# Optimization experiments

Hardware: AMD Instinct MI355X
Metric: run time of the kernel (lower is better)

The kernel has to match this reference:

```python
import jax, jax.numpy as jnp
import numpy as np

S, B, H = 2048, 16, 512      # seq_len, batch, hidden_size
L = 4096                     # total labels across batch
SMAX = 16                    # max span length
LAB = 256                    # label_size
V = 32000                    # len(voc)


def setup_inputs() -> dict:
    key = jax.random.key(0)
    ks = jax.random.split(key, 10)
    hidden = jax.random.normal(ks[0], (S, B, H), jnp.float32)
    begins = jax.random.randint(ks[1], (L,), 1, S - SMAX - 1)          # >=1 so begin-1 valid
    lens = jax.random.randint(ks[2], (L,), 1, SMAX + 1)                # span length in [1, SMAX]
    ends = begins + lens                                               # < S so hidden[end] valid
    bids = jax.random.randint(ks[3], (L,), 0, B)
    tags = jax.random.randint(ks[4], (L,), 0, V)
    sc = 0.02
    W1 = jax.random.normal(ks[5], (3 * H, LAB), jnp.float32) * sc
    b1 = jnp.zeros((LAB,), jnp.float32)
    W2 = jax.random.normal(ks[6], (LAB, LAB), jnp.float32) * sc
    b2 = jnp.zeros((LAB,), jnp.float32)
    Wo = jax.random.normal(ks[7], (LAB, V), jnp.float32) * sc
    bo = jnp.zeros((V,), jnp.float32)
    return dict(hidden=hidden, begins=begins, ends=ends, bids=bids, tags=tags,
                W1=W1, b1=b1, W2=W2, b2=b2, Wo=Wo, bo=bo)


def reference(hidden, begins, ends, bids, tags, W1, b1, W2, b2, Wo, bo):
    # --- batched span embed: gather + masked mean + boundary concat ---
    pos = begins[:, None] + jnp.arange(SMAX)            # [L, SMAX]
    valid = (pos < ends[:, None]).astype(hidden.dtype)  # [L, SMAX]
    posc = jnp.minimum(pos, S - 1)
    g = hidden[posc, bids[:, None]]                     # [L, SMAX, H] gather
    span_len = (ends - begins).astype(hidden.dtype)[:, None]
    mean = (g * valid[..., None]).sum(axis=1) / span_len           # [L, H]
    left = hidden[begins - 1, bids]                                 # [L, H]
    right = hidden[ends, bids]                                      # [L, H]
    span_emb = jnp.concatenate([left, mean, right], axis=-1)        # [L, 3H]
    # --- hidden2feature: Linear -> sigmoid -> Linear (dropout = eval identity) ---
    feat = jax.nn.sigmoid(span_emb @ W1 + b1) @ W2 + b2             # [L, LAB]
    # --- SoftmaxLoss: -log_softmax(h2o(feat)).gather(tags).mean() per label ---
    logp = jax.nn.log_softmax(feat @ Wo + bo, axis=-1)              # [L, V]
    per_label = -logp[jnp.arange(L), tags]                          # one tag per label
    return per_label.sum() / (L + 1e-5)
```

## Files before the change

kernel.cpp:

```cpp
#include <hip/hip_runtime.h>
#include <math.h>

#define S 2048
#define B 16
#define H 512
#define L 4096
#define SMAX 16
#define LAB 256
#define V 32000
#define NCH 250
#define LOG2E 1.44269504f

typedef __attribute__((ext_vector_type(8))) short short8;
typedef __attribute__((ext_vector_type(4))) float float4v;

__device__ inline ushort f2bf(float x) {
  union { float f; unsigned u; } c; c.f = x;
  unsigned r = c.u + 0x7fffu + ((c.u >> 16) & 1u);
  return (ushort)(r >> 16);
}
__device__ inline float bf2f(ushort h) {
  union { unsigned u; float f; } c; c.u = ((unsigned)h) << 16;
  return c.f;
}

__global__ __launch_bounds__(256) void spanb_kernel(
    const float* __restrict__ hidden, const int* __restrict__ begins,
    const int* __restrict__ ends, const int* __restrict__ bids,
    ushort* __restrict__ spanb) {
  int sub = threadIdx.x >> 7, t = threadIdx.x & 127;
  int l = blockIdx.x * 2 + sub;
  int b = bids[l], s0 = begins[l], s1 = ends[l];
  const float4* hidv = (const float4*)hidden;
  float4 lf = hidv[((size_t)(s0 - 1) * B + b) * 128 + t];
  float4 rf = hidv[((size_t)s1 * B + b) * 128 + t];
  float4 m = make_float4(0.f, 0.f, 0.f, 0.f);
  int len = s1 - s0;
  for (int j = 0; j < len; ++j) {
    float4 g = hidv[((size_t)(s0 + j) * B + b) * 128 + t];
    m.x += g.x; m.y += g.y; m.z += g.z; m.w += g.w;
  }
  float inv = 1.0f / (float)len;
  ushort* sp = spanb + (size_t)l * 1536;
  ushort4 u;
  u.x = f2bf(lf.x); u.y = f2bf(lf.y); u.z = f2bf(lf.z); u.w = f2bf(lf.w);
  *(ushort4*)&sp[t * 4] = u;
  u.x = f2bf(m.x * inv); u.y = f2bf(m.y * inv);
  u.z = f2bf(m.z * inv); u.w = f2bf(m.w * inv);
  *(ushort4*)&sp[512 + t * 4] = u;
  u.x = f2bf(rf.x); u.y = f2bf(rf.y); u.z = f2bf(rf.z); u.w = f2bf(rf.w);
  *(ushort4*)&sp[1024 + t * 4] = u;
}

__global__ __launch_bounds__(256) void tcast_kernel(
    const float* __restrict__ src, ushort* __restrict__ dst, int K, int N) {
  __shared__ ushort tile[64 * 72];
  int t = threadIdx.x;
  int n0 = blockIdx.x * 64;
  int k0 = blockIdx.y * 64;
  #pragma unroll
  for (int p = 0; p < 16; ++p) {
    int k = p * 4 + (t >> 6);
    int n = t & 63;
    tile[n * 72 + k] = f2bf(src[(size_t)(k0 + k) * N + n0 + n]);
  }
  __syncthreads();
  #pragma unroll
  for (int p = 0; p < 2; ++p) {
    int idx = p * 256 + t;
    int n = idx >> 3, c = idx & 7;
    *(uint4*)&dst[(size_t)(n0 + n) * K + k0 + c * 8] =
        *(const uint4*)&tile[n * 72 + c * 8];
  }
}

#define FST 72
__global__ __launch_bounds__(256, 2) void feat_mfma_kernel(
    const ushort* __restrict__ spanb, const ushort* __restrict__ W1b,
    const float* __restrict__ b1, const ushort* __restrict__ W2b,
    const float* __restrict__ b2, ushort* __restrict__ featb) {
  __shared__ ushort As[32 * FST];
  __shared__ ushort Bs[256 * FST];
  __shared__ ushort Hs[32 * 264];
  int tid = threadIdx.x;
  int w = tid >> 6, lane = tid & 63;
  int lr = lane & 15, lq = lane >> 4;
  int l0 = blockIdx.x * 32;

  float4v acc[2][4];
  float4v zero = {0.f, 0.f, 0.f, 0.f};
  #pragma unroll
  for (int mt = 0; mt < 2; ++mt)
    #pragma unroll
    for (int nt = 0; nt < 4; ++nt) acc[mt][nt] = zero;

  for (int s = 0; s < 24; ++s) {
    int ks = s * 64;
    __syncthreads();
    {
      int r = tid >> 3, c = tid & 7;
      *(uint4*)&As[r * FST + c * 8] =
          *(const uint4*)&spanb[(size_t)(l0 + r) * 1536 + ks + c * 8];
    }
    #pragma unroll
    for (int p = 0; p < 8; ++p) {
      int idx = p * 256 + tid;
      int r = idx >> 3, c = idx & 7;
      *(uint4*)&Bs[r * FST + c * 8] =
          *(const uint4*)&W1b[(size_t)r * 1536 + ks + c * 8];
    }
    __syncthreads();
    #pragma unroll
    for (int kk = 0; kk < 2; ++kk) {
      short8 af[2], bf[4];
      #pragma unroll
      for (int mt = 0; mt < 2; ++mt)
        af[mt] = *(const short8*)&As[(mt * 16 + lr) * FST + kk * 32 + lq * 8];
      #pragma unroll
      for (int nt = 0; nt < 4; ++nt)
        bf[nt] = *(const short8*)
            &Bs[(w * 64 + nt * 16 + lr) * FST + kk * 32 + lq * 8];
      #pragma unroll
      for (int mt = 0; mt < 2; ++mt)
        #pragma unroll
        for (int nt = 0; nt < 4; ++nt)
          acc[mt][nt] = __builtin_amdgcn_mfma_f32_16x16x32_bf16(
              af[mt], bf[nt], acc[mt][nt], 0, 0, 0);
    }
  }

  {
    float b1v[4];
    #pragma unroll
    for (int nt = 0; nt < 4; ++nt) b1v[nt] = b1[w * 64 + nt * 16 + lr];
    #pragma unroll
    for (int mt = 0; mt < 2; ++mt)
      #pragma unroll
      for (int nt = 0; nt < 4; ++nt)
        #pragma unroll
        for (int r = 0; r < 4; ++r) {
          int row = mt * 16 + lq * 4 + r;
          int col = w * 64 + nt * 16 + lr;
          float h = 1.0f / (1.0f + __expf(-(acc[mt][nt][r] + b1v[nt])));
          Hs[row * 264 + col] = f2bf(h);
        }
  }

  float4v acc2[2][4];
  #pragma unroll
  for (int mt = 0; mt < 2; ++mt)
    #pragma unroll
    for (int nt = 0; nt < 4; ++nt) acc2[mt][nt] = zero;

  for (int s = 0; s < 4; ++s) {
    int ks = s * 64;
    __syncthreads();
    #pragma unroll
    for (int p = 0; p < 8; ++p) {
      int idx = p * 256 + tid;
      int r = idx >> 3, c = idx & 7;
      *(uint4*)&Bs[r * FST + c * 8] =
          *(const uint4*)&W2b[(size_t)r * 256 + ks + c * 8];
    }
    __syncthreads();
    #pragma unroll
    for (int kk = 0; kk < 2; ++kk) {
      short8 af[2], bf[4];
      #pragma unroll
      for (int mt = 0; mt < 2; ++mt)
        af[mt] = *(const short8*)
            &Hs[(mt * 16 + lr) * 264 + ks + kk * 32 + lq * 8];
      #pragma unroll
      for (int nt = 0; nt < 4; ++nt)
        bf[nt] = *(const short8*)
            &Bs[(w * 64 + nt * 16 + lr) * FST + kk * 32 + lq * 8];
      #pragma unroll
      for (int mt = 0; mt < 2; ++mt)
        #pragma unroll
        for (int nt = 0; nt < 4; ++nt)
          acc2[mt][nt] = __builtin_amdgcn_mfma_f32_16x16x32_bf16(
              af[mt], bf[nt], acc2[mt][nt], 0, 0, 0);
    }
  }

  {
    float b2v[4];
    #pragma unroll
    for (int nt = 0; nt < 4; ++nt) b2v[nt] = b2[w * 64 + nt * 16 + lr];
    #pragma unroll
    for (int mt = 0; mt < 2; ++mt)
      #pragma unroll
      for (int nt = 0; nt < 4; ++nt)
        #pragma unroll
        for (int r = 0; r < 4; ++r) {
          int row = mt * 16 + lq * 4 + r;
          int col = w * 64 + nt * 16 + lr;
          featb[(size_t)(l0 + row) * 256 + col] =
              f2bf(acc2[mt][nt][r] + b2v[nt]);
        }
  }
}

#define BST2 264
__global__ __launch_bounds__(256, 2) void logits2_kernel(
    const ushort* __restrict__ featb, const ushort* __restrict__ Wob,
    const float* __restrict__ bo, float* __restrict__ pz) {
  __shared__ ushort Blds[128 * BST2];
  int tid = threadIdx.x;
  int l0 = blockIdx.x * 256;
  int v0 = blockIdx.y * 128;
  int w = tid >> 6, lane = tid & 63;
  int lr = lane & 15, lq = lane >> 4;

  {
    const uint4* src = (const uint4*)(Wob + (size_t)v0 * 256);
    #pragma unroll
    for (int p = 0; p < 16; ++p) {
      int idx = p * 256 + tid;
      int r = idx >> 5, c = idx & 31;
      *(uint4*)&Blds[r * BST2 + c * 8] = src[idx];
    }
  }
  __syncthreads();

  const short8* aptr[4];
  #pragma unroll
  for (int mt = 0; mt < 4; ++mt)
    aptr[mt] = (const short8*)(featb +
        (size_t)(l0 + w * 64 + mt * 16 + lr) * 256 + lq * 8);

  float4v acc[4][8];
  float4v zero = {0.f, 0.f, 0.f, 0.f};
  #pragma unroll
  for (int mt = 0; mt < 4; ++mt)
    #pragma unroll
    for (int nt = 0; nt < 8; ++nt) acc[mt][nt] = zero;

  short8 af[2][4];
  #pragma unroll
  for (int mt = 0; mt < 4; ++mt) af[0][mt] = aptr[mt][0];

  #pragma unroll
  for (int k = 0; k < 8; ++k) {
    int cur = k & 1, nxt = cur ^ 1;
    if (k < 7) {
      #pragma unroll
      for (int mt = 0; mt < 4; ++mt)
        af[nxt][mt] = aptr[mt][(k + 1) * 2];
    }
    short8 bf[8];
    #pragma unroll
    for (int nt = 0; nt < 8; ++nt)
      bf[nt] = *(const short8*)&Blds[(nt * 16 + lr) * BST2 + k * 32 + lq * 8];
    #pragma unroll
    for (int mt = 0; mt < 4; ++mt)
      #pragma unroll
      for (int nt = 0; nt < 8; ++nt)
        acc[mt][nt] = __builtin_amdgcn_mfma_f32_16x16x32_bf16(
            af[cur][mt], bf[nt], acc[mt][nt], 0, 0, 0);
  }

  float bov[8];
  #pragma unroll
  for (int nt = 0; nt < 8; ++nt)
    bov[nt] = bo[v0 + nt * 16 + lr] * LOG2E;
  float z[4][4];
  #pragma unroll
  for (int mt = 0; mt < 4; ++mt)
    #pragma unroll
    for (int r = 0; r < 4; ++r) z[mt][r] = 0.f;
  #pragma unroll
  for (int mt = 0; mt < 4; ++mt)
    #pragma unroll
    for (int nt = 0; nt < 8; ++nt)
      #pragma unroll
      for (int r = 0; r < 4; ++r)
        z[mt][r] += exp2f(fmaf(acc[mt][nt][r], LOG2E, bov[nt]));
  #pragma unroll
  for (int mt = 0; mt < 4; ++mt)
    #pragma unroll
    for (int r = 0; r < 4; ++r) {
      #pragma unroll
      for (int off = 1; off < 16; off <<= 1)
        z[mt][r] += __shfl_xor(z[mt][r], off);
    }
  if (lr == 0) {
    int ch = blockIdx.y;
    #pragma unroll
    for (int mt = 0; mt < 4; ++mt)
      #pragma unroll
      for (int r = 0; r < 4; ++r)
        pz[(size_t)ch * L + l0 + w * 64 + mt * 16 + lq * 4 + r] = z[mt][r];
  }
}

__global__ __launch_bounds__(256) void tag_kernel(
    const ushort* __restrict__ featb, const ushort* __restrict__ Wob,
    const float* __restrict__ bo, const int* __restrict__ tags,
    float* __restrict__ tagl) {
  int l = blockIdx.x * 4 + (threadIdx.x >> 6);
  int lane = threadIdx.x & 63;
  int tg = tags[l];
  ushort4 fa = *(const ushort4*)&featb[(size_t)l * 256 + lane * 4];
  ushort4 wa = *(const ushort4*)&Wob[(size_t)tg * 256 + lane * 4];
  float s = bf2f(fa.x) * bf2f(wa.x) + bf2f(fa.y) * bf2f(wa.y) +
            bf2f(fa.z) * bf2f(wa.z) + bf2f(fa.w) * bf2f(wa.w);
  #pragma unroll
  for (int off = 1; off < 64; off <<= 1) s += __shfl_xor(s, off);
  if (lane == 0) tagl[l] = s + bo[tg];
}

__global__ __launch_bounds__(256) void reduce_kernel(
    const float* __restrict__ pz, const float* __restrict__ tagl,
    float* __restrict__ out) {
  int l = blockIdx.x * 256 + threadIdx.x;
  float z = 0.f;
  for (int c = 0; c < NCH; ++c) z += pz[(size_t)c * L + l];
  float per = logf(z) - tagl[l];
  float v = per * (1.0f / (4096.0f + 1e-5f));
  #pragma unroll
  for (int off = 1; off < 64; off <<= 1) v += __shfl_xor(v, off);
  __shared__ float wsum[4];
  if ((threadIdx.x & 63) == 0) wsum[threadIdx.x >> 6] = v;
  __syncthreads();
  if (threadIdx.x == 0)
    atomicAdd(out, wsum[0] + wsum[1] + wsum[2] + wsum[3]);
}

extern "C" void kernel_launch(void* const* d_in, const int* in_sizes, int n_in,
                              void* d_out, int out_size, void* d_ws,
                              size_t ws_size, hipStream_t stream) {
  const float* hidden = (const float*)d_in[0];
  const int* begins = (const int*)d_in[1];
  const int* ends = (const int*)d_in[2];
  const int* bids = (const int*)d_in[3];
  const int* tags = (const int*)d_in[4];
  const float* W1 = (const float*)d_in[5];
  const float* b1 = (const float*)d_in[6];
  const float* W2 = (const float*)d_in[7];
  const float* b2 = (const float*)d_in[8];
  const float* Wo = (const float*)d_in[9];
  const float* bo = (const float*)d_in[10];
  float* out = (float*)d_out;

  ushort* featb = (ushort*)d_ws;
  ushort* Wob = featb + (size_t)L * 256;
  ushort* spanb = Wob + (size_t)V * 256;
  ushort* W1b = spanb + (size_t)L * 1536;
  ushort* W2b = W1b + (size_t)256 * 1536;
  float* pz = (float*)(W2b + (size_t)256 * 256);
  float* tagl = pz + (size_t)NCH * L;

  hipMemsetAsync(d_out, 0, sizeof(float), stream);
  spanb_kernel<<<L / 2, 256, 0, stream>>>(hidden, begins, ends, bids, spanb);
  tcast_kernel<<<dim3(4, 24), 256, 0, stream>>>(W1, W1b, 1536, LAB);
  tcast_kernel<<<dim3(4, 4), 256, 0, stream>>>(W2, W2b, LAB, LAB);
  tcast_kernel<<<dim3(500, 4), 256, 0, stream>>>(Wo, Wob, LAB, V);
  feat_mfma_kernel<<<128, 256, 0, stream>>>(spanb, W1b, b1, W2b, b2, featb);
  logits2_kernel<<<dim3(16, NCH), 256, 0, stream>>>(featb, Wob, bo, pz);
  tag_kernel<<<L / 4, 256, 0, stream>>>(featb, Wob, bo, tags, tagl);
  reduce_kernel<<<L / 256, 256, 0, stream>>>(pz, tagl, out);
}
```

Baseline: 314.0 us.

## Pre-swizzle Wo into MFMA fragment order and stream it with direct-to-LDS loads

The Wo bf16 cast kernel now writes the weights directly in the MFMA B-fragment order for each 128-column chunk. This lets the logits kernel load them with global_load_lds in two K halves, with no padded LDS layout and conflict-free fragment reads. The logits tile shrinks to 128 rows per block, which doubles the grid and uses half the LDS to allow three blocks per CU, and s_setprio is wrapped around the MFMA bursts. The tag kernel is updated to index the swizzled layout, and pz reuses the spanb workspace buffer, which is safe only because spanb is dead once the feat kernel has run. In exchange, each B tile is reused by fewer rows, so more weight data is loaded per output.

```diff
diff --git a/kernel.cpp b/kernel.cpp
--- a/kernel.cpp
+++ b/kernel.cpp
@@ -74,6 +74,31 @@
   }
 }
 
+__global__ __launch_bounds__(256) void tcast_wo_kernel(
+    const float* __restrict__ src, ushort* __restrict__ dst) {
+  __shared__ ushort tile[64 * 72];
+  int t = threadIdx.x;
+  int n0 = blockIdx.x * 64;
+  int k0 = blockIdx.y * 64;
+  #pragma unroll
+  for (int p = 0; p < 16; ++p) {
+    int k = p * 4 + (t >> 6);
+    int n = t & 63;
+    tile[n * 72 + k] = f2bf(src[(size_t)(k0 + k) * V + n0 + n]);
+  }
+  __syncthreads();
+  #pragma unroll
+  for (int p = 0; p < 2; ++p) {
+    int idx = p * 256 + t;
+    int n = idx >> 3, c8 = idx & 7;
+    int v = n0 + n, k = k0 + c8 * 8;
+    int c = v >> 7, nt = (v >> 4) & 7, lr = v & 15;
+    int kh = k >> 7, k4 = (k >> 5) & 3, lq = (k >> 3) & 3;
+    size_t f = ((((size_t)c * 2 + kh) * 4 + k4) * 8 + nt) * 64 + lq * 16 + lr;
+    *(uint4*)&dst[f * 8] = *(const uint4*)&tile[n * 72 + c8 * 8];
+  }
+}
+
 #define FST 72
 __global__ __launch_bounds__(256, 2) void feat_mfma_kernel(
     const ushort* __restrict__ spanb, const ushort* __restrict__ W1b,
@@ -201,83 +226,92 @@
   }
 }
 
-#define BST2 264
-__global__ __launch_bounds__(256, 2) void logits2_kernel(
+__global__ __launch_bounds__(256, 3) void logits2_kernel(
     const ushort* __restrict__ featb, const ushort* __restrict__ Wob,
     const float* __restrict__ bo, float* __restrict__ pz) {
-  __shared__ ushort Blds[128 * BST2];
+  __shared__ ushort Blds[16384];
   int tid = threadIdx.x;
-  int l0 = blockIdx.x * 256;
-  int v0 = blockIdx.y * 128;
   int w = tid >> 6, lane = tid & 63;
   int lr = lane & 15, lq = lane >> 4;
-
-  {
-    const uint4* src = (const uint4*)(Wob + (size_t)v0 * 256);
-    #pragma unroll
-    for (int p = 0; p < 16; ++p) {
-      int idx = p * 256 + tid;
-      int r = idx >> 5, c = idx & 31;
-      *(uint4*)&Blds[r * BST2 + c * 8] = src[idx];
-    }
-  }
-  __syncthreads();
-
-  const short8* aptr[4];
-  #pragma unroll
-  for (int mt = 0; mt < 4; ++mt)
+  int l0 = blockIdx.x * 128;
+  int v0 = blockIdx.y * 128;
+
+  const short8* aptr[2];
+  #pragma unroll
+  for (int mt = 0; mt < 2; ++mt)
     aptr[mt] = (const short8*)(featb +
-        (size_t)(l0 + w * 64 + mt * 16 + lr) * 256 + lq * 8);
-
-  float4v acc[4][8];
-  float4v zero = {0.f, 0.f, 0.f, 0.f};
-  #pragma unroll
-  for (int mt = 0; mt < 4; ++mt)
-    #pragma unroll
-    for (int nt = 0; nt < 8; ++nt) acc[mt][nt] = zero;
-
-  short8 af[2][4];
-  #pragma unroll
-  for (int mt = 0; mt < 4; ++mt) af[0][mt] = aptr[mt][0];
-
-  #pragma unroll
-  for (int k = 0; k < 8; ++k) {
-    int cur = k & 1, nxt = cur ^ 1;
-    if (k < 7) {
-      #pragma unroll
-      for (int mt = 0; mt < 4; ++mt)
-        af[nxt][mt] = aptr[mt][(k + 1) * 2];
-    }
-    short8 bf[8];
-    #pragma unroll
-    for (int nt = 0; nt < 8; ++nt)
-      bf[nt] = *(const short8*)&Blds[(nt * 16 + lr) * BST2 + k * 32 + lq * 8];
-    #pragma unroll
-    for (int mt = 0; mt < 4; ++mt)
-      #pragma unroll
-      for (int nt = 0; nt < 8; ++nt)
-        acc[mt][nt] = __builtin_amdgcn_mfma_f32_16x16x32_bf16(
-            af[cur][mt], bf[nt], acc[mt][nt], 0, 0, 0);
-  }
+        (size_t)(l0 + w * 32 + mt * 16 + lr) * 256 + lq * 8);
 
   float bov[8];
   #pragma unroll
   for (int nt = 0; nt < 8; ++nt)
     bov[nt] = bo[v0 + nt * 16 + lr] * LOG2E;
-  float z[4][4];
-  #pragma unroll
-  for (int mt = 0; mt < 4; ++mt)
+
+  float4v acc[2][8];
+  float4v zero = {0.f, 0.f, 0.f, 0.f};
+  #pragma unroll
+  for (int mt = 0; mt < 2; ++mt)
+    #pragma unroll
+    for (int nt = 0; nt < 8; ++nt) acc[mt][nt] = zero;
+
+  short8 af[2][2];
+  #pragma unroll
+  for (int mt = 0; mt < 2; ++mt) af[0][mt] = aptr[mt][0];
+
+  #pragma unroll
+  for (int kh = 0; kh < 2; ++kh) {
+    {
+      const uint4* src4 = (const uint4*)(Wob +
+          (size_t)blockIdx.y * 32768 + (size_t)kh * 16384);
+      #pragma unroll
+      for (int p = 0; p < 8; ++p) {
+        int idx = p * 256 + tid;
+        __builtin_amdgcn_global_load_lds(
+            (const __attribute__((address_space(1))) unsigned int*)(src4 + idx),
+            (__attribute__((address_space(3))) unsigned int*)&Blds[(size_t)idx * 8],
+            16, 0, 0);
+      }
+    }
+    __syncthreads();
+    #pragma unroll
+    for (int k4 = 0; k4 < 4; ++k4) {
+      int kg = kh * 4 + k4;
+      int cur = kg & 1, nxt = cur ^ 1;
+      if (kg < 7) {
+        #pragma unroll
+        for (int mt = 0; mt < 2; ++mt)
+          af[nxt][mt] = aptr[mt][(kg + 1) * 4];
+      }
+      short8 bf[8];
+      #pragma unroll
+      for (int nt = 0; nt < 8; ++nt)
+        bf[nt] = *(const short8*)&Blds[(size_t)(((k4 * 8 + nt) * 64) + lane) * 8];
+      __builtin_amdgcn_s_setprio(1);
+      #pragma unroll
+      for (int mt = 0; mt < 2; ++mt)
+        #pragma unroll
+        for (int nt = 0; nt < 8; ++nt)
+          acc[mt][nt] = __builtin_amdgcn_mfma_f32_16x16x32_bf16(
+              af[cur][mt], bf[nt], acc[mt][nt], 0, 0, 0);
+      __builtin_amdgcn_s_setprio(0);
+    }
+    if (kh == 0) __syncthreads();
+  }
+
+  float z[2][4];
+  #pragma unroll
+  for (int mt = 0; mt < 2; ++mt)
     #pragma unroll
     for (int r = 0; r < 4; ++r) z[mt][r] = 0.f;
   #pragma unroll
-  for (int mt = 0; mt < 4; ++mt)
+  for (int mt = 0; mt < 2; ++mt)
     #pragma unroll
     for (int nt = 0; nt < 8; ++nt)
       #pragma unroll
       for (int r = 0; r < 4; ++r)
         z[mt][r] += exp2f(fmaf(acc[mt][nt][r], LOG2E, bov[nt]));
   #pragma unroll
-  for (int mt = 0; mt < 4; ++mt)
+  for (int mt = 0; mt < 2; ++mt)
     #pragma unroll
     for (int r = 0; r < 4; ++r) {
       #pragma unroll
@@ -287,10 +321,11 @@
   if (lr == 0) {
     int ch = blockIdx.y;
     #pragma unroll
-    for (int mt = 0; mt < 4; ++mt)
-      #pragma unroll
-      for (int r = 0; r < 4; ++r)
-        pz[(size_t)ch * L + l0 + w * 64 + mt * 16 + lq * 4 + r] = z[mt][r];
+    for (int mt = 0; mt < 2; ++mt) {
+      float4 v4;
+      v4.x = z[mt][0]; v4.y = z[mt][1]; v4.z = z[mt][2]; v4.w = z[mt][3];
+      *(float4*)&pz[(size_t)ch * L + l0 + w * 32 + mt * 16 + lq * 4] = v4;
+    }
   }
 }
 
@@ -301,8 +336,12 @@
   int l = blockIdx.x * 4 + (threadIdx.x >> 6);
   int lane = threadIdx.x & 63;
   int tg = tags[l];
-  ushort4 fa = *(const ushort4*)&featb[(size_t)l * 256 + lane * 4];
-  ushort4 wa = *(const ushort4*)&Wob[(size_t)tg * 256 + lane * 4];
+  int c = tg >> 7, nt = (tg >> 4) & 7, lr = tg & 15;
+  int k0 = lane << 2;
+  int kh = k0 >> 7, k4 = (k0 >> 5) & 3, lq = (k0 >> 3) & 3, e = k0 & 7;
+  size_t f = ((((size_t)c * 2 + kh) * 4 + k4) * 8 + nt) * 64 + lq * 16 + lr;
+  ushort4 wa = *(const ushort4*)&Wob[f * 8 + e];
+  ushort4 fa = *(const ushort4*)&featb[(size_t)l * 256 + k0];
   float s = bf2f(fa.x) * bf2f(wa.x) + bf2f(fa.y) * bf2f(wa.y) +
             bf2f(fa.z) * bf2f(wa.z) + bf2f(fa.w) * bf2f(wa.w);
   #pragma unroll
@@ -348,16 +387,16 @@
   ushort* spanb = Wob + (size_t)V * 256;
   ushort* W1b = spanb + (size_t)L * 1536;
   ushort* W2b = W1b + (size_t)256 * 1536;
-  float* pz = (float*)(W2b + (size_t)256 * 256);
-  float* tagl = pz + (size_t)NCH * L;
+  float* pz = (float*)spanb;
+  float* tagl = (float*)(W2b + (size_t)256 * 256);
 
   hipMemsetAsync(d_out, 0, sizeof(float), stream);
   spanb_kernel<<<L / 2, 256, 0, stream>>>(hidden, begins, ends, bids, spanb);
   tcast_kernel<<<dim3(4, 24), 256, 0, stream>>>(W1, W1b, 1536, LAB);
   tcast_kernel<<<dim3(4, 4), 256, 0, stream>>>(W2, W2b, LAB, LAB);
-  tcast_kernel<<<dim3(500, 4), 256, 0, stream>>>(Wo, Wob, LAB, V);
+  tcast_wo_kernel<<<dim3(500, 4), 256, 0, stream>>>(Wo, Wob);
   feat_mfma_kernel<<<128, 256, 0, stream>>>(spanb, W1b, b1, W2b, b2, featb);
-  logits2_kernel<<<dim3(16, NCH), 256, 0, stream>>>(featb, Wob, bo, pz);
+  logits2_kernel<<<dim3(32, NCH), 256, 0, stream>>>(featb, Wob, bo, pz);
   tag_kernel<<<L / 4, 256, 0, stream>>>(featb, Wob, bo, tags, tagl);
   reduce_kernel<<<L / 256, 256, 0, stream>>>(pz, tagl, out);
 }
```

New measurement: 290.4 us. 7.5% less time.
